# Optimization experiments

Hardware: AMD Instinct MI355X
Metric: run time of the kernel (lower is better)

## Reference

```python
import jax, jax.numpy as jnp
import numpy as np

TAU = 0.07
LAMBDA_RN = 1.0
LAMBDA_U = 1.0
BETA_FLOOR = 0.0
PRIOR_W = 0.1
PHASE1_END = 5
PHASE2_END = 15
B = 8192
NEG = -1e30  # finite stand-in for -inf (safe gradients)


def setup_inputs() -> dict:
    key = jax.random.key(0)
    ks = jax.random.split(key, 7)
    return {
        "sim_matrix": jax.random.normal(ks[0], (B, B), jnp.float32),
        "pu_labels": jax.random.randint(ks[1], (B,), 0, 3, jnp.int32) - 1,  # {-1,0,1}
        "alphas": jax.random.uniform(ks[2], (B,), jnp.float32),
        "betas": jax.random.uniform(ks[3], (B,), jnp.float32),
        "pi_a": jax.random.uniform(ks[4], (B,), jnp.float32),
        "pu_weights": jax.random.uniform(ks[5], (B,), jnp.float32)[:, None] * jnp.ones((1, B), jnp.float32) * 0 + jax.random.uniform(ks[5], (B, B), jnp.float32),
        "pi_a_external": jax.random.uniform(ks[6], (B,), jnp.float32),
        "epoch": 20,
    }


def _infonce(logits):
    n = logits.shape[0]
    idx = jnp.arange(n)
    la = -jnp.mean(jax.nn.log_softmax(logits, axis=1)[idx, idx])
    lc = -jnp.mean(jax.nn.log_softmax(logits.T, axis=1)[idx, idx])
    return (la + lc) / 2.0


def _pu_loss(logits, pu_labels, alphas, betas, pi_a, pu_weights):
    n = logits.shape[0]
    other = ~jnp.eye(n, dtype=bool)                      # exclude self
    log_Z = jax.nn.logsumexp(jnp.where(other, logits, NEG), axis=1)  # (B,)
    rel = logits - log_Z[:, None]                        # (B,B) logits - logZ
    e = jnp.exp(rel)                                     # exp(logit - logZ)

    p = pu_labels == 1
    rn = pu_labels == -1
    u = pu_labels == 0
    pos_m = other & p[None, :]
    rn_m = other & rn[None, :]
    u_m = other & u[None, :]
    c_pos = pos_m.sum(1)
    c_rn = rn_m.sum(1)
    c_u = u_m.sum(1)

    L_pos = -jnp.where(pos_m, alphas[None, :] * rel, 0.0).sum(1) / jnp.maximum(c_pos, 1)
    L_rn = jnp.where(rn_m, betas[None, :] * pu_weights * e, 0.0).sum(1) / jnp.maximum(c_rn, 1)

    E_U = jnp.where(u_m, pu_weights * e, 0.0).sum(1) / jnp.maximum(c_u, 1)
    E_P = jnp.where(pos_m, e, 0.0).sum(1) / jnp.maximum(c_pos, 1)
    pi = jnp.clip(pi_a, 1e-4, 0.5)
    debiased = (E_U - pi * E_P) / (1.0 - pi + 1e-8)
    L_u = jnp.where((c_u > 0) & (c_pos > 0), jnp.maximum(debiased, BETA_FLOOR), 0.0)

    L_pos = jnp.where(c_pos > 0, L_pos, 0.0)
    L_rn = jnp.where(c_rn > 0, L_rn, 0.0)
    return jnp.mean(L_pos + LAMBDA_RN * L_rn + LAMBDA_U * L_u)


def reference(sim_matrix, pu_labels, alphas, betas, pi_a, pu_weights, pi_a_external, epoch):
    logits = sim_matrix / TAU
    loss_infonce = _infonce(logits)
    # curriculum (epoch is a static Python int)
    if epoch < PHASE1_END:
        return loss_infonce
    pu_w = 1.0 if epoch >= PHASE2_END else (epoch - PHASE1_END) / max(PHASE2_END - PHASE1_END, 1)
    loss_pu = _pu_loss(logits, pu_labels, alphas, betas, pi_a, pu_weights)
    total = (1.0 - pu_w) * loss_infonce + pu_w * loss_pu
    if epoch >= PHASE2_END:  # phase 3 with pi_a_external provided
        total = total + PRIOR_W * jnp.mean((pi_a - pi_a_external) ** 2)
    return total
```

## Files before the change

kernel.cpp:

```cpp
#include <hip/hip_runtime.h>
#include <hip/hip_fp16.h>
#include <math.h>

#define BN 8192
#define NT 256
#define NW (NT / 64)
#define NGRP 8
#define INV_TAU (1.0f / 0.07f)
#define COFF 40.0f

struct WsLayout {
  double bins_pu[64];
  double bins_ir[64];
  double bins_ic[64];
  double acc_prior;
  float w_inf, w_pu, w_prior;
  int P_tot, RN_tot, U_tot;
  float A_tot;
};

__global__ void prep_kernel(const int* __restrict__ labels, const float* __restrict__ alphas,
                            const float* __restrict__ betas, const float* __restrict__ pia,
                            const float* __restrict__ pie, const int* __restrict__ epoch_p,
                            WsLayout* __restrict__ ws, __half2* __restrict__ code) {
  const int t = threadIdx.x;
  __shared__ int sP[1024], sRN[1024], sU[1024];
  __shared__ float sA[1024], sPr[1024];
  int p = 0, rn = 0, u = 0;
  float a = 0.f, pr = 0.f;
  for (int j = t; j < BN; j += 1024) {
    const int l = labels[j];
    const bool isp = (l == 1), isrn = (l == -1);
    p += isp; rn += isrn; u += (l == 0);
    const __half vh = __float2half(isp ? alphas[j] : (isrn ? betas[j] : 0.f));
    const __half ch = __float2half(isp ? 1.f : (isrn ? -1.f : 0.f));
    code[j] = __halves2half2(vh, ch);
    a += isp ? __half2float(vh) : 0.f;
    const float d = pia[j] - pie[j];
    pr = fmaf(d, d, pr);
  }
  sP[t] = p; sRN[t] = rn; sU[t] = u; sA[t] = a; sPr[t] = pr;
  __syncthreads();
  for (int s = 512; s > 0; s >>= 1) {
    if (t < s) {
      sP[t] += sP[t + s]; sRN[t] += sRN[t + s]; sU[t] += sU[t + s];
      sA[t] += sA[t + s]; sPr[t] += sPr[t + s];
    }
    __syncthreads();
  }
  if (t < 64) { ws->bins_pu[t] = 0.0; ws->bins_ir[t] = 0.0; ws->bins_ic[t] = 0.0; }
  if (t == 0) {
    ws->acc_prior = (double)sPr[0];
    ws->P_tot = sP[0]; ws->RN_tot = sRN[0]; ws->U_tot = sU[0]; ws->A_tot = sA[0];
    const int ep = epoch_p[0];
    float w_inf, w_pu, w_prior;
    if (ep < 5) { w_inf = 1.f; w_pu = 0.f; w_prior = 0.f; }
    else {
      const float puw = (ep >= 15) ? 1.f : (float)(ep - 5) / 10.f;
      w_inf = 1.f - puw; w_pu = puw; w_prior = (ep >= 15) ? 1.f : 0.f;
    }
    ws->w_inf = w_inf; ws->w_pu = w_pu; ws->w_prior = w_prior;
  }
}

__launch_bounds__(NT, 4)
__global__ void row_kernel(const float* __restrict__ sim, const float* __restrict__ pw,
                           const __half2* __restrict__ code, const float* __restrict__ pia,
                           WsLayout* __restrict__ ws) {
  const int row = blockIdx.x;
  const float w_pu = ws->w_pu, w_inf = ws->w_inf;
  if (w_pu == 0.0f && w_inf == 0.0f) return;
  const bool do_pu = (w_pu != 0.0f);

  const float4* __restrict__ sim4 = (const float4*)(sim + (size_t)row * BN);
  const float4* __restrict__ cd4  = (const float4*)code;
  const float4* __restrict__ pwp  = do_pu ? (const float4*)(pw + (size_t)row * BN) : sim4;

  float se = 0.f, sp = 0.f, srn = 0.f, su = 0.f, sas = 0.f;

#pragma unroll
  for (int it = 0; it < NGRP; ++it) {
    const int v = threadIdx.x + it * NT;
    const float4 s4 = sim4[v];
    const float4 w4 = pwp[v];
    const float4 c4 = cd4[v];
    const float sv[4] = {s4.x, s4.y, s4.z, s4.w};
    const float wv[4] = {w4.x, w4.y, w4.z, w4.w};
    const float cf[4] = {c4.x, c4.y, c4.z, c4.w};
#pragma unroll
    for (int c = 0; c < 4; ++c) {
      const __half2 h = __builtin_bit_cast(__half2, cf[c]);
      const float2 f = __half22float2(h);
      const float s = sv[c];
      const float ex = __expf(fmaf(s, INV_TAU, -COFF));
      se += ex;
      const bool isp  = f.y > 0.5f;
      const bool isrn = f.y < -0.5f;
      sp += isp ? ex : 0.f;
      const float we = wv[c] * ex;
      srn = fmaf(isrn ? f.x : 0.f, we, srn);
      su += (f.y == 0.f) ? we : 0.f;
      sas = fmaf(isp ? f.x : 0.f, s, sas);
    }
  }

  const int wid = threadIdx.x >> 6;
  const int lane = threadIdx.x & 63;
#pragma unroll
  for (int off = 32; off > 0; off >>= 1) {
    se  += __shfl_xor(se, off);
    sp  += __shfl_xor(sp, off);
    srn += __shfl_xor(srn, off);
    su  += __shfl_xor(su, off);
    sas += __shfl_xor(sas, off);
  }
  __shared__ float red[NW][8];
  if (lane == 0) {
    red[wid][0] = se; red[wid][1] = sp; red[wid][2] = srn;
    red[wid][3] = su; red[wid][4] = sas;
  }
  __syncthreads();

  if (threadIdx.x == 0) {
    double Se = 0.0, Sp = 0.0, Sr = 0.0, Su = 0.0, Sa = 0.0;
#pragma unroll
    for (int w = 0; w < NW; ++w) {
      Se += (double)red[w][0]; Sp += (double)red[w][1]; Sr += (double)red[w][2];
      Su += (double)red[w][3]; Sa += (double)red[w][4];
    }
    const float s_rr = sim[(size_t)row * BN + row];
    const float l_rr = s_rr * INV_TAU;
    const float ex_rr_f = __expf(fmaf(s_rr, INV_TAU, -COFF));
    const double ex_rr = (double)ex_rr_f;
    const float2 fr = __half22float2(code[row]);
    const bool rp = fr.y > 0.5f, rrn = fr.y < -0.5f, ru = (fr.y == 0.f);
    const float asr = rp ? fr.x : 0.f;
    const float rbr = rrn ? fr.x : 0.f;

    const double se_ex = fmax(Se - ex_rr, 1e-300);
    const double logZ = (double)COFF + log(se_ex);

    if (do_pu) {
      const float pw_rr = pw[(size_t)row * BN + row];
      const int cp  = ws->P_tot  - (rp ? 1 : 0);
      const int crn = ws->RN_tot - (rrn ? 1 : 0);
      const int cu  = ws->U_tot  - (ru ? 1 : 0);
      const double Apos  = (double)ws->A_tot - (double)asr;
      const double SaL   = (double)INV_TAU * Sa - (double)asr * (double)l_rr;
      const double sp_ex = Sp - (rp ? ex_rr : 0.0);
      const double sr_ex = Sr - (double)rbr * (double)pw_rr * ex_rr;
      const double su_ex = Su - (ru ? (double)pw_rr * ex_rr : 0.0);

      const double Lpos = (cp > 0) ? (-(SaL - logZ * Apos) / cp) : 0.0;
      const double Lrn  = (crn > 0) ? ((sr_ex / se_ex) / crn) : 0.0;
      const double EU = (su_ex / se_ex) / (cu > 0 ? cu : 1);
      const double EP = (sp_ex / se_ex) / (cp > 0 ? cp : 1);
      double pi = (double)pia[row];
      pi = pi < 1e-4 ? 1e-4 : (pi > 0.5 ? 0.5 : pi);
      const double deb = (EU - pi * EP) / (1.0 - pi + 1e-8);
      const double Lu = (cu > 0 && cp > 0) ? (deb > 0.0 ? deb : 0.0) : 0.0;
      atomicAdd(&ws->bins_pu[row & 63], Lpos + Lrn + Lu);
    }
    if (w_inf != 0.0f) {
      const double logZf = (double)COFF + log(Se);
      atomicAdd(&ws->bins_ir[row & 63], logZf - (double)l_rr);
    }
  }
}

#define COLS_PER_BLK 8
__launch_bounds__(256)
__global__ void col_kernel(const float* __restrict__ sim, WsLayout* __restrict__ ws) {
  if (ws->w_inf == 0.0f) return;
  for (int k = 0; k < COLS_PER_BLK; ++k) {
    const int col = blockIdx.x * COLS_PER_BLK + k;
    float m = -3.0e38f, se = 0.f, diag = 0.f;
    for (int r = threadIdx.x; r < BN; r += 256) {
      const float l = sim[(size_t)r * BN + col] * INV_TAU;
      if (r == col) diag = l;
      if (l > m) { se *= __expf(m - l); m = l; }
      se += __expf(l - m);
    }
#pragma unroll
    for (int off = 32; off > 0; off >>= 1) {
      const float m2 = __shfl_xor(m, off), se2 = __shfl_xor(se, off);
      diag += __shfl_xor(diag, off);
      const float mn = fmaxf(m, m2);
      se = se * __expf(m - mn) + se2 * __expf(m2 - mn);
      m = mn;
    }
    __shared__ float red[4][3];
    const int wid = threadIdx.x >> 6;
    const int lane = threadIdx.x & 63;
    if (lane == 0) { red[wid][0] = m; red[wid][1] = se; red[wid][2] = diag; }
    __syncthreads();
    if (threadIdx.x == 0) {
      float M = red[0][0], Se = red[0][1], Dg = red[0][2];
      for (int w = 1; w < 4; ++w) {
        const float mn = fmaxf(M, red[w][0]);
        Se = Se * __expf(M - mn) + red[w][1] * __expf(red[w][0] - mn);
        M = mn;
        Dg += red[w][2];
      }
      const double logZf = (double)M + log((double)Se);
      atomicAdd(&ws->bins_ic[col & 63], logZf - (double)Dg);
    }
    __syncthreads();
  }
}

__global__ void final_kernel(const WsLayout* __restrict__ ws, float* __restrict__ out) {
  const int t = threadIdx.x;
  double pu = ws->bins_pu[t];
  double ir = ws->bins_ir[t];
  double ic = ws->bins_ic[t];
#pragma unroll
  for (int off = 32; off > 0; off >>= 1) {
    pu += __shfl_xor(pu, off);
    ir += __shfl_xor(ir, off);
    ic += __shfl_xor(ic, off);
  }
  if (t == 0) {
    const double loss_pu  = pu / (double)BN;
    const double loss_inf = (ir + ic) / (2.0 * (double)BN);
    const double prior    = ws->acc_prior / (double)BN;
    const double total = (double)ws->w_inf * loss_inf
                       + (double)ws->w_pu * loss_pu
                       + (double)ws->w_prior * 0.1 * prior;
    out[0] = (float)total;
  }
}

extern "C" void kernel_launch(void* const* d_in, const int* in_sizes, int n_in,
                              void* d_out, int out_size, void* d_ws, size_t ws_size,
                              hipStream_t stream) {
  const float* sim    = (const float*)d_in[0];
  const int*   labels = (const int*)d_in[1];
  const float* alphas = (const float*)d_in[2];
  const float* betas  = (const float*)d_in[3];
  const float* pia    = (const float*)d_in[4];
  const float* pw     = (const float*)d_in[5];
  const float* pie    = (const float*)d_in[6];
  const int*   epoch  = (const int*)d_in[7];
  WsLayout* ws = (WsLayout*)d_ws;
  __half2* code = (__half2*)((char*)d_ws + 4096);
  float* out = (float*)d_out;

  hipLaunchKernelGGL(prep_kernel, dim3(1), dim3(1024), 0, stream,
                     labels, alphas, betas, pia, pie, epoch, ws, code);
  hipLaunchKernelGGL(row_kernel, dim3(BN), dim3(NT), 0, stream,
                     sim, pw, code, pia, ws);
  hipLaunchKernelGGL(col_kernel, dim3(BN / COLS_PER_BLK), dim3(256), 0, stream, sim, ws);
  hipLaunchKernelGGL(final_kernel, dim3(1), dim3(64), 0, stream, ws, out);
}
```

Measured before the change: 119.6 us.

## Vectorize prep loads, batch row loads, widen row blocks, resize column grid

Result: faster. 113.8 us (-4.8%).

```diff
diff --git a/kernel.cpp b/kernel.cpp
--- a/kernel.cpp
+++ b/kernel.cpp
@@ -3,9 +3,9 @@
 #include <math.h>
 
 #define BN 8192
-#define NT 256
+#define NT 512
 #define NW (NT / 64)
-#define NGRP 8
+#define NGRP 4
 #define INV_TAU (1.0f / 0.07f)
 #define COFF 40.0f
 
@@ -24,26 +24,46 @@
                             const float* __restrict__ pie, const int* __restrict__ epoch_p,
                             WsLayout* __restrict__ ws, __half2* __restrict__ code) {
   const int t = threadIdx.x;
-  __shared__ int sP[1024], sRN[1024], sU[1024];
+  __shared__ int sP[1024], sRN[1024];
   __shared__ float sA[1024], sPr[1024];
-  int p = 0, rn = 0, u = 0;
+  int p = 0, rn = 0;
   float a = 0.f, pr = 0.f;
-  for (int j = t; j < BN; j += 1024) {
-    const int l = labels[j];
-    const bool isp = (l == 1), isrn = (l == -1);
-    p += isp; rn += isrn; u += (l == 0);
-    const __half vh = __float2half(isp ? alphas[j] : (isrn ? betas[j] : 0.f));
-    const __half ch = __float2half(isp ? 1.f : (isrn ? -1.f : 0.f));
-    code[j] = __halves2half2(vh, ch);
-    a += isp ? __half2float(vh) : 0.f;
-    const float d = pia[j] - pie[j];
-    pr = fmaf(d, d, pr);
-  }
-  sP[t] = p; sRN[t] = rn; sU[t] = u; sA[t] = a; sPr[t] = pr;
+  const int4*   lb4 = (const int4*)labels;
+  const float4* al4 = (const float4*)alphas;
+  const float4* be4 = (const float4*)betas;
+  const float4* pa4 = (const float4*)pia;
+  const float4* pe4 = (const float4*)pie;
+#pragma unroll
+  for (int g = 0; g < BN / 4 / 1024; ++g) {
+    const int v = t + g * 1024;
+    const int4 l4 = lb4[v];
+    const float4 a4 = al4[v];
+    const float4 b4 = be4[v];
+    const float4 x4 = pa4[v];
+    const float4 e4 = pe4[v];
+    const int lv[4] = {l4.x, l4.y, l4.z, l4.w};
+    const float av[4] = {a4.x, a4.y, a4.z, a4.w};
+    const float bv[4] = {b4.x, b4.y, b4.z, b4.w};
+    const float xv[4] = {x4.x, x4.y, x4.z, x4.w};
+    const float ev[4] = {e4.x, e4.y, e4.z, e4.w};
+#pragma unroll
+    for (int c = 0; c < 4; ++c) {
+      const int l = lv[c];
+      const bool isp = (l == 1), isrn = (l == -1);
+      p += isp; rn += isrn;
+      const __half vh = __float2half(isp ? av[c] : (isrn ? bv[c] : 0.f));
+      const __half ch = __float2half(isp ? 1.f : (isrn ? -1.f : 0.f));
+      code[4 * v + c] = __halves2half2(vh, ch);
+      a += isp ? __half2float(vh) : 0.f;
+      const float d = xv[c] - ev[c];
+      pr = fmaf(d, d, pr);
+    }
+  }
+  sP[t] = p; sRN[t] = rn; sA[t] = a; sPr[t] = pr;
   __syncthreads();
   for (int s = 512; s > 0; s >>= 1) {
     if (t < s) {
-      sP[t] += sP[t + s]; sRN[t] += sRN[t + s]; sU[t] += sU[t + s];
+      sP[t] += sP[t + s]; sRN[t] += sRN[t + s];
       sA[t] += sA[t + s]; sPr[t] += sPr[t + s];
     }
     __syncthreads();
@@ -51,7 +71,9 @@
   if (t < 64) { ws->bins_pu[t] = 0.0; ws->bins_ir[t] = 0.0; ws->bins_ic[t] = 0.0; }
   if (t == 0) {
     ws->acc_prior = (double)sPr[0];
-    ws->P_tot = sP[0]; ws->RN_tot = sRN[0]; ws->U_tot = sU[0]; ws->A_tot = sA[0];
+    ws->P_tot = sP[0]; ws->RN_tot = sRN[0];
+    ws->U_tot = BN - sP[0] - sRN[0];
+    ws->A_tot = sA[0];
     const int ep = epoch_p[0];
     float w_inf, w_pu, w_prior;
     if (ep < 5) { w_inf = 1.f; w_pu = 0.f; w_prior = 0.f; }
@@ -76,17 +98,20 @@
   const float4* __restrict__ cd4  = (const float4*)code;
   const float4* __restrict__ pwp  = do_pu ? (const float4*)(pw + (size_t)row * BN) : sim4;
 
+  float4 s4[NGRP], w4[NGRP], c4[NGRP];
+#pragma unroll
+  for (int it = 0; it < NGRP; ++it) s4[it] = sim4[threadIdx.x + it * NT];
+#pragma unroll
+  for (int it = 0; it < NGRP; ++it) w4[it] = pwp[threadIdx.x + it * NT];
+#pragma unroll
+  for (int it = 0; it < NGRP; ++it) c4[it] = cd4[threadIdx.x + it * NT];
+
   float se = 0.f, sp = 0.f, srn = 0.f, su = 0.f, sas = 0.f;
-
 #pragma unroll
   for (int it = 0; it < NGRP; ++it) {
-    const int v = threadIdx.x + it * NT;
-    const float4 s4 = sim4[v];
-    const float4 w4 = pwp[v];
-    const float4 c4 = cd4[v];
-    const float sv[4] = {s4.x, s4.y, s4.z, s4.w};
-    const float wv[4] = {w4.x, w4.y, w4.z, w4.w};
-    const float cf[4] = {c4.x, c4.y, c4.z, c4.w};
+    const float sv[4] = {s4[it].x, s4[it].y, s4[it].z, s4[it].w};
+    const float wv[4] = {w4[it].x, w4[it].y, w4[it].z, w4[it].w};
+    const float cf[4] = {c4[it].x, c4[it].y, c4[it].z, c4[it].w};
 #pragma unroll
     for (int c = 0; c < 4; ++c) {
       const __half2 h = __builtin_bit_cast(__half2, cf[c]);
@@ -168,7 +193,8 @@
   }
 }
 
-#define COLS_PER_BLK 8
+#define COL_BLKS 256
+#define COLS_PER_BLK (BN / COL_BLKS)
 __launch_bounds__(256)
 __global__ void col_kernel(const float* __restrict__ sim, WsLayout* __restrict__ ws) {
   if (ws->w_inf == 0.0f) return;
@@ -250,6 +276,6 @@
                      labels, alphas, betas, pia, pie, epoch, ws, code);
   hipLaunchKernelGGL(row_kernel, dim3(BN), dim3(NT), 0, stream,
                      sim, pw, code, pia, ws);
-  hipLaunchKernelGGL(col_kernel, dim3(BN / COLS_PER_BLK), dim3(256), 0, stream, sim, ws);
+  hipLaunchKernelGGL(col_kernel, dim3(COL_BLKS), dim3(256), 0, stream, sim, ws);
   hipLaunchKernelGGL(final_kernel, dim3(1), dim3(64), 0, stream, ws, out);
 }
```

## Parallelize prep, batch row loads, simplify label encoding, rebalance column grid

Applied to the files above, without the earlier changes.

Result: slower. 123.1 us (+3.0%).

```diff
diff --git a/kernel.cpp b/kernel.cpp
--- a/kernel.cpp
+++ b/kernel.cpp
@@ -8,50 +8,47 @@
 #define NGRP 8
 #define INV_TAU (1.0f / 0.07f)
 #define COFF 40.0f
+#define K2F 20.609929065f
+#define C2F 57.707801636f
 
 struct WsLayout {
   double bins_pu[64];
   double bins_ir[64];
   double bins_ic[64];
   double acc_prior;
+  int P_tot, RN_tot;
+  float A_tot;
   float w_inf, w_pu, w_prior;
-  int P_tot, RN_tot, U_tot;
-  float A_tot;
 };
 
 __global__ void prep_kernel(const int* __restrict__ labels, const float* __restrict__ alphas,
                             const float* __restrict__ betas, const float* __restrict__ pia,
                             const float* __restrict__ pie, const int* __restrict__ epoch_p,
                             WsLayout* __restrict__ ws, __half2* __restrict__ code) {
-  const int t = threadIdx.x;
-  __shared__ int sP[1024], sRN[1024], sU[1024];
-  __shared__ float sA[1024], sPr[1024];
-  int p = 0, rn = 0, u = 0;
-  float a = 0.f, pr = 0.f;
-  for (int j = t; j < BN; j += 1024) {
-    const int l = labels[j];
-    const bool isp = (l == 1), isrn = (l == -1);
-    p += isp; rn += isrn; u += (l == 0);
-    const __half vh = __float2half(isp ? alphas[j] : (isrn ? betas[j] : 0.f));
-    const __half ch = __float2half(isp ? 1.f : (isrn ? -1.f : 0.f));
-    code[j] = __halves2half2(vh, ch);
-    a += isp ? __half2float(vh) : 0.f;
-    const float d = pia[j] - pie[j];
-    pr = fmaf(d, d, pr);
-  }
-  sP[t] = p; sRN[t] = rn; sU[t] = u; sA[t] = a; sPr[t] = pr;
-  __syncthreads();
-  for (int s = 512; s > 0; s >>= 1) {
-    if (t < s) {
-      sP[t] += sP[t + s]; sRN[t] += sRN[t + s]; sU[t] += sU[t + s];
-      sA[t] += sA[t + s]; sPr[t] += sPr[t + s];
-    }
-    __syncthreads();
-  }
-  if (t < 64) { ws->bins_pu[t] = 0.0; ws->bins_ir[t] = 0.0; ws->bins_ic[t] = 0.0; }
-  if (t == 0) {
-    ws->acc_prior = (double)sPr[0];
-    ws->P_tot = sP[0]; ws->RN_tot = sRN[0]; ws->U_tot = sU[0]; ws->A_tot = sA[0];
+  const int j = blockIdx.x * 256 + threadIdx.x;
+  const int l = labels[j];
+  const bool isp = (l == 1), isrn = (l == -1);
+  const float v = isp ? alphas[j] : (isrn ? -betas[j] : 0.f);
+  const __half vh = __float2half(v);
+  code[j] = __halves2half2(vh, __float2half((!isp && !isrn) ? 1.f : 0.f));
+  int p = isp ? 1 : 0, rn = isrn ? 1 : 0;
+  float a = isp ? __half2float(vh) : 0.f;
+  const float d = pia[j] - pie[j];
+  float pr = d * d;
+#pragma unroll
+  for (int off = 32; off > 0; off >>= 1) {
+    p  += __shfl_xor(p, off);
+    rn += __shfl_xor(rn, off);
+    a  += __shfl_xor(a, off);
+    pr += __shfl_xor(pr, off);
+  }
+  if ((threadIdx.x & 63) == 0) {
+    atomicAdd(&ws->P_tot, p);
+    atomicAdd(&ws->RN_tot, rn);
+    atomicAdd(&ws->A_tot, a);
+    atomicAdd(&ws->acc_prior, (double)pr);
+  }
+  if (blockIdx.x == 0 && threadIdx.x == 0) {
     const int ep = epoch_p[0];
     float w_inf, w_pu, w_prior;
     if (ep < 5) { w_inf = 1.f; w_pu = 0.f; w_prior = 0.f; }
@@ -63,7 +60,7 @@
   }
 }
 
-__launch_bounds__(NT, 4)
+__launch_bounds__(NT, 3)
 __global__ void row_kernel(const float* __restrict__ sim, const float* __restrict__ pw,
                            const __half2* __restrict__ code, const float* __restrict__ pia,
                            WsLayout* __restrict__ ws) {
@@ -76,31 +73,33 @@
   const float4* __restrict__ cd4  = (const float4*)code;
   const float4* __restrict__ pwp  = do_pu ? (const float4*)(pw + (size_t)row * BN) : sim4;
 
-  float se = 0.f, sp = 0.f, srn = 0.f, su = 0.f, sas = 0.f;
-
+  float4 s4[NGRP], w4[NGRP], c4[NGRP];
 #pragma unroll
   for (int it = 0; it < NGRP; ++it) {
     const int v = threadIdx.x + it * NT;
-    const float4 s4 = sim4[v];
-    const float4 w4 = pwp[v];
-    const float4 c4 = cd4[v];
-    const float sv[4] = {s4.x, s4.y, s4.z, s4.w};
-    const float wv[4] = {w4.x, w4.y, w4.z, w4.w};
-    const float cf[4] = {c4.x, c4.y, c4.z, c4.w};
+    s4[it] = sim4[v];
+    w4[it] = pwp[v];
+    c4[it] = cd4[v];
+  }
+
+  float se = 0.f, sp = 0.f, srn = 0.f, su = 0.f, sas = 0.f;
+#pragma unroll
+  for (int it = 0; it < NGRP; ++it) {
+    const float sv[4] = {s4[it].x, s4[it].y, s4[it].z, s4[it].w};
+    const float wv[4] = {w4[it].x, w4[it].y, w4[it].z, w4[it].w};
+    const float cf[4] = {c4[it].x, c4[it].y, c4[it].z, c4[it].w};
 #pragma unroll
     for (int c = 0; c < 4; ++c) {
       const __half2 h = __builtin_bit_cast(__half2, cf[c]);
       const float2 f = __half22float2(h);
       const float s = sv[c];
-      const float ex = __expf(fmaf(s, INV_TAU, -COFF));
+      const float ex = exp2f(fmaf(s, K2F, -C2F));
       se += ex;
-      const bool isp  = f.y > 0.5f;
-      const bool isrn = f.y < -0.5f;
-      sp += isp ? ex : 0.f;
       const float we = wv[c] * ex;
-      srn = fmaf(isrn ? f.x : 0.f, we, srn);
-      su += (f.y == 0.f) ? we : 0.f;
-      sas = fmaf(isp ? f.x : 0.f, s, sas);
+      sp += (f.x > 0.f) ? ex : 0.f;
+      su  = fmaf(f.y, we, su);
+      srn = fmaf(fmaxf(-f.x, 0.f), we, srn);
+      sas = fmaf(fmaxf(f.x, 0.f), s, sas);
     }
   }
 
@@ -130,21 +129,23 @@
     }
     const float s_rr = sim[(size_t)row * BN + row];
     const float l_rr = s_rr * INV_TAU;
-    const float ex_rr_f = __expf(fmaf(s_rr, INV_TAU, -COFF));
+    const float ex_rr_f = exp2f(fmaf(s_rr, K2F, -C2F));
     const double ex_rr = (double)ex_rr_f;
     const float2 fr = __half22float2(code[row]);
-    const bool rp = fr.y > 0.5f, rrn = fr.y < -0.5f, ru = (fr.y == 0.f);
-    const float asr = rp ? fr.x : 0.f;
-    const float rbr = rrn ? fr.x : 0.f;
+    const bool rp = fr.x > 0.f, rrn = fr.x < 0.f, ru = fr.y > 0.5f;
+    const float asr = fmaxf(fr.x, 0.f);
+    const float rbr = fmaxf(-fr.x, 0.f);
 
     const double se_ex = fmax(Se - ex_rr, 1e-300);
     const double logZ = (double)COFF + log(se_ex);
 
     if (do_pu) {
       const float pw_rr = pw[(size_t)row * BN + row];
-      const int cp  = ws->P_tot  - (rp ? 1 : 0);
-      const int crn = ws->RN_tot - (rrn ? 1 : 0);
-      const int cu  = ws->U_tot  - (ru ? 1 : 0);
+      const int P_tot = ws->P_tot, RN_tot = ws->RN_tot;
+      const int U_tot = BN - P_tot - RN_tot;
+      const int cp  = P_tot  - (rp ? 1 : 0);
+      const int crn = RN_tot - (rrn ? 1 : 0);
+      const int cu  = U_tot  - (ru ? 1 : 0);
       const double Apos  = (double)ws->A_tot - (double)asr;
       const double SaL   = (double)INV_TAU * Sa - (double)asr * (double)l_rr;
       const double sp_ex = Sp - (rp ? ex_rr : 0.0);
@@ -168,7 +169,8 @@
   }
 }
 
-#define COLS_PER_BLK 8
+#define COL_BLKS 256
+#define COLS_PER_BLK (BN / COL_BLKS)
 __launch_bounds__(256)
 __global__ void col_kernel(const float* __restrict__ sim, WsLayout* __restrict__ ws) {
   if (ws->w_inf == 0.0f) return;
@@ -246,10 +248,11 @@
   __half2* code = (__half2*)((char*)d_ws + 4096);
   float* out = (float*)d_out;
 
-  hipLaunchKernelGGL(prep_kernel, dim3(1), dim3(1024), 0, stream,
+  hipMemsetAsync(d_ws, 0, 2048, stream);
+  hipLaunchKernelGGL(prep_kernel, dim3(32), dim3(256), 0, stream,
                      labels, alphas, betas, pia, pie, epoch, ws, code);
   hipLaunchKernelGGL(row_kernel, dim3(BN), dim3(NT), 0, stream,
                      sim, pw, code, pia, ws);
-  hipLaunchKernelGGL(col_kernel, dim3(BN / COLS_PER_BLK), dim3(256), 0, stream, sim, ws);
+  hipLaunchKernelGGL(col_kernel, dim3(COL_BLKS), dim3(256), 0, stream, sim, ws);
   hipLaunchKernelGGL(final_kernel, dim3(1), dim3(64), 0, stream, ws, out);
 }
```
